# Kernel optimization log

Measured on AMD Instinct MI355X. Metric: run time of the kernel, lower is better.

## Reference

```python
import jax, jax.numpy as jnp
import numpy as np
from jax import lax

KS = 3
N = KS ** 3  # 27 kernel taps


def setup_inputs() -> dict:
    key = jax.random.key(0)
    k1, k2, k3 = jax.random.split(key, 3)
    B, Cin, Cout, D, H, W = 1, 32, 32, 32, 48, 48
    x = jax.random.normal(k1, (B, Cin, D, H, W), jnp.float32)
    # offset conv: 81 = 3*27 output channels, no bias (nn.Conv3d(..., bias=False))
    w_off = jax.random.normal(k2, (3 * N, Cin, KS, KS, KS), jnp.float32) * 0.01
    # deform conv kernel (bias defaults to None -> no bias)
    w_def = jax.random.normal(k3, (Cout, Cin, KS, KS, KS), jnp.float32) / np.sqrt(Cin * N)
    return {"x": x, "w_off": w_off, "w_def": w_def}


def _deform_block(x, w_off, w_def):
    B, C, D, H, W = x.shape
    dt = x.dtype

    # standard dense offset conv, padding=1
    offsets = lax.conv_general_dilated(
        x, w_off, (1, 1, 1), [(1, 1), (1, 1), (1, 1)],
        dimension_numbers=("NCDHW", "OIDHW", "NCDHW"))
    off = jnp.transpose(offsets, (0, 2, 3, 4, 1))  # (B,D,H,W,3N)
    od, oh, ow = off[..., :N], off[..., N:2 * N], off[..., 2 * N:]

    # zero-pad input (ConstantPad3d(1))
    xp = jnp.pad(x, ((0, 0), (0, 0), (1, 1), (1, 1), (1, 1)))
    Dp, Hp, Wp = D + 2, H + 2, W + 2

    # p_n: kernel grid offsets in (kd,kh,kw) row-major order, matching conv-weight layout
    r = jnp.arange(-(KS // 2), KS // 2 + 1, dtype=dt)
    pn = jnp.stack(jnp.meshgrid(r, r, r, indexing="ij"), 0).reshape(3, N)
    # p_0: centers in padded coordinates (1..D etc.)
    p0d = jnp.arange(1, D + 1, dtype=dt)[:, None, None, None]
    p0h = jnp.arange(1, H + 1, dtype=dt)[None, :, None, None]
    p0w = jnp.arange(1, W + 1, dtype=dt)[None, None, :, None]

    pd = p0d + pn[0] + od  # (B,D,H,W,N) sampling coords
    ph = p0h + pn[1] + oh
    pw = p0w + pn[2] + ow

    # integer corners (detached in original)
    fd = lax.stop_gradient(jnp.floor(pd))
    fh = lax.stop_gradient(jnp.floor(ph))
    fw = lax.stop_gradient(jnp.floor(pw))
    qd0 = jnp.clip(fd, 0, Dp - 1); qd1 = jnp.clip(fd + 1, 0, Dp - 1)
    qh0 = jnp.clip(fh, 0, Hp - 1); qh1 = jnp.clip(fh + 1, 0, Hp - 1)
    qw0 = jnp.clip(fw, 0, Wp - 1); qw1 = jnp.clip(fw + 1, 0, Wp - 1)

    # clip p to valid range (as in reference impl)
    pd = jnp.clip(pd, 0, Dp - 1)
    ph = jnp.clip(ph, 0, Hp - 1)
    pw = jnp.clip(pw, 0, Wp - 1)

    # trilinear weights per axis: g = 1 - |q - p|
    gd0 = 1 + (qd0 - pd); gd1 = 1 - (qd1 - pd)
    gh0 = 1 + (qh0 - ph); gh1 = 1 - (qh1 - ph)
    gw0 = 1 + (qw0 - pw); gw1 = 1 - (qw1 - pw)

    xf = xp.reshape(B, C, Dp * Hp * Wp)

    def gather(idd, ihh, iww):
        lin = ((idd.astype(jnp.int32) * Hp + ihh.astype(jnp.int32)) * Wp
               + iww.astype(jnp.int32)).reshape(B, 1, -1)
        v = jnp.take_along_axis(xf, jnp.broadcast_to(lin, (B, C, lin.shape[-1])), axis=2)
        return v.reshape(B, C, D, H, W, N)

    x_off = jnp.zeros((B, C, D, H, W, N), dt)
    for gd, idd in ((gd0, qd0), (gd1, qd1)):
        for gh, ihh in ((gh0, qh0), (gh1, qh1)):
            for gw, iww in ((gw0, qw0), (gw1, qw1)):
                x_off = x_off + (gd * gh * gw)[:, None] * gather(idd, ihh, iww)

    # stride-ks conv over reshaped x_offset == weighted sum over the N taps
    Cout = w_def.shape[0]
    out = jnp.einsum("bcdhwn,ocn->bodhw", x_off, w_def.reshape(Cout, C, N))
    return out


def reference(x, w_off, w_def):
    return _deform_block(x, w_off, w_def)
```

## Files before the change

### kernel.cpp

```cpp
#include <hip/hip_runtime.h>

typedef __attribute__((ext_vector_type(8))) short  short8;
typedef __attribute__((ext_vector_type(4))) float  f32x4;
typedef __attribute__((ext_vector_type(2))) float  f32x2;

#define CIN 32
#define COUT 32
#define DD 32
#define HH 48
#define WW 48
#define NTAP 27
#define SPATIAL (DD*HH*WW)

#define BP2_ELEMS (27*6*64*8)
#define OFF_WPK   ((size_t)BP2_ELEMS*2)
#define WPK_ELEMS (27*2*64*8)
#define OFF_XT    (OFF_WPK + (size_t)WPK_ELEMS*2)

#define SB0() __builtin_amdgcn_sched_barrier(0)

__device__ __forceinline__ unsigned short f2bf(float f) {
    union { float f; unsigned u; } v; v.f = f;
    unsigned r = v.u + 0x7FFFu + ((v.u >> 16) & 1u);
    return (unsigned short)(r >> 16);
}
__device__ __forceinline__ float bitsf(unsigned u) {
    union { unsigned u; float f; } v; v.u = u; return v.f;
}

__global__ __launch_bounds__(256) void wprep2_kernel(
        const float* __restrict__ w_off, unsigned short* __restrict__ Bp2)
{
    int i = blockIdx.x * 256 + threadIdx.x;
    if (i >= BP2_ELEMS) return;
    int e    = i & 7;
    int lane = (i >> 3) & 63;
    int j    = (i >> 9) % 6;
    int n    = i / (512 * 6);
    int col = lane & 15, kg = lane >> 4;
    int oc = j * 16 + col, c = kg * 8 + e;
    float v = (oc < 81) ? w_off[((size_t)oc * CIN + c) * NTAP + n] : 0.f;
    Bp2[i] = f2bf(v);
}

__global__ __launch_bounds__(256) void wdefprep_kernel(
        const float* __restrict__ w_def, unsigned short* __restrict__ wpk)
{
    int i = blockIdx.x * 256 + threadIdx.x;
    if (i >= WPK_ELEMS) return;
    int e    = i & 7;
    int lane = (i >> 3) & 63;
    int half = (i >> 9) & 1;
    int n    = i >> 10;
    int kg = lane >> 4, col = lane & 15;
    int c  = kg * 8 + e, oc = half * 16 + col;
    wpk[i] = f2bf(w_def[((size_t)oc * CIN + c) * NTAP + n]);
}

__global__ __launch_bounds__(256) void xtrans_kernel(
        const float* __restrict__ x, unsigned short* __restrict__ xT)
{
    __shared__ float t[CIN][65];
    const int p0 = blockIdx.x * 64;
    const int tid = threadIdx.x;
    const int tx = tid & 63, ty = tid >> 6;
    #pragma unroll
    for (int k = 0; k < 8; ++k) {
        int c = ty + k * 4;
        t[c][tx] = x[(size_t)c * SPATIAL + p0 + tx];
    }
    __syncthreads();
    const int pl = tid >> 2, cg = (tid & 3) * 8;
    short8 v;
    #pragma unroll
    for (int i = 0; i < 8; ++i) v[i] = (short)f2bf(t[cg + i][pl]);
    *(short8*)&xT[((size_t)(p0 + pl)) * 32 + cg] = v;
}

struct Gath {
    uint4 cw[8];
    float gg[8];
};

__device__ __forceinline__ void tap_issue(
        Gath& tb, const uint4* __restrict__ Xu,
        float od, float oh, float ow,
        int n, int d, int h, int w, int kg)
{
    float rd = (float)(n / 9) - 1.f;
    float rh = (float)((n / 3) % 3) - 1.f;
    float rw = (float)(n % 3) - 1.f;

    float pdp = (float)(d + 1) + rd + od;
    float php = (float)(h + 1) + rh + oh;
    float pwp = (float)(w + 1) + rw + ow;

    float fd = floorf(pdp), fh = floorf(php), fw = floorf(pwp);
    float qd0 = fminf(fmaxf(fd,       0.f), 33.f);
    float qd1 = fminf(fmaxf(fd + 1.f, 0.f), 33.f);
    float qh0 = fminf(fmaxf(fh,       0.f), 49.f);
    float qh1 = fminf(fmaxf(fh + 1.f, 0.f), 49.f);
    float qw0 = fminf(fmaxf(fw,       0.f), 49.f);
    float qw1 = fminf(fmaxf(fw + 1.f, 0.f), 49.f);
    float pcd = fminf(fmaxf(pdp, 0.f), 33.f);
    float pch = fminf(fmaxf(php, 0.f), 49.f);
    float pcw = fminf(fmaxf(pwp, 0.f), 49.f);

    float gd0 = 1.f + (qd0 - pcd), gd1 = 1.f - (qd1 - pcd);
    float gh0 = 1.f + (qh0 - pch), gh1 = 1.f - (qh1 - pch);
    float gw0 = 1.f + (qw0 - pcw), gw1 = 1.f - (qw1 - pcw);
    gd0 = (qd0 >= 1.f && qd0 <= 32.f) ? gd0 : 0.f;
    gd1 = (qd1 >= 1.f && qd1 <= 32.f) ? gd1 : 0.f;
    gh0 = (qh0 >= 1.f && qh0 <= 48.f) ? gh0 : 0.f;
    gh1 = (qh1 >= 1.f && qh1 <= 48.f) ? gh1 : 0.f;
    gw0 = (qw0 >= 1.f && qw0 <= 48.f) ? gw0 : 0.f;
    gw1 = (qw1 >= 1.f && qw1 <= 48.f) ? gw1 : 0.f;
    int zd0 = (int)fminf(fmaxf(qd0, 1.f), 32.f) - 1;
    int zd1 = (int)fminf(fmaxf(qd1, 1.f), 32.f) - 1;
    int zh0 = (int)fminf(fmaxf(qh0, 1.f), 48.f) - 1;
    int zh1 = (int)fminf(fmaxf(qh1, 1.f), 48.f) - 1;
    int zw0 = (int)fminf(fmaxf(qw0, 1.f), 48.f) - 1;
    int zw1 = (int)fminf(fmaxf(qw1, 1.f), 48.f) - 1;

    int bd0 = zd0 * 2304, bd1 = zd1 * 2304;
    int bh0 = zh0 * 48,   bh1 = zh1 * 48;
    float gdh00 = gd0 * gh0, gdh01 = gd0 * gh1;
    float gdh10 = gd1 * gh0, gdh11 = gd1 * gh1;

    tb.cw[0] = Xu[(size_t)(bd0 + bh0 + zw0) * 4 + kg];
    tb.cw[1] = Xu[(size_t)(bd0 + bh0 + zw1) * 4 + kg];
    tb.cw[2] = Xu[(size_t)(bd0 + bh1 + zw0) * 4 + kg];
    tb.cw[3] = Xu[(size_t)(bd0 + bh1 + zw1) * 4 + kg];
    tb.cw[4] = Xu[(size_t)(bd1 + bh0 + zw0) * 4 + kg];
    tb.cw[5] = Xu[(size_t)(bd1 + bh0 + zw1) * 4 + kg];
    tb.cw[6] = Xu[(size_t)(bd1 + bh1 + zw0) * 4 + kg];
    tb.cw[7] = Xu[(size_t)(bd1 + bh1 + zw1) * 4 + kg];

    tb.gg[0] = gdh00 * gw0;  tb.gg[1] = gdh00 * gw1;
    tb.gg[2] = gdh01 * gw0;  tb.gg[3] = gdh01 * gw1;
    tb.gg[4] = gdh10 * gw0;  tb.gg[5] = gdh10 * gw1;
    tb.gg[6] = gdh11 * gw0;  tb.gg[7] = gdh11 * gw1;
}

__device__ __forceinline__ void tap_consume(
        const Gath& tb, short8 b0, short8 b1, f32x4& acc0, f32x4& acc1)
{
    f32x2 xa0 = {0.f, 0.f}, xa1 = {0.f, 0.f};
    f32x2 xa2 = {0.f, 0.f}, xa3 = {0.f, 0.f};

    #pragma unroll
    for (int e = 0; e < 8; ++e) {
        uint4 cw = tb.cw[e];
        f32x2 g2 = {tb.gg[e], tb.gg[e]};
        f32x2 v0 = {bitsf(cw.x << 16), bitsf(cw.x & 0xFFFF0000u)};
        f32x2 v1 = {bitsf(cw.y << 16), bitsf(cw.y & 0xFFFF0000u)};
        f32x2 v2 = {bitsf(cw.z << 16), bitsf(cw.z & 0xFFFF0000u)};
        f32x2 v3 = {bitsf(cw.w << 16), bitsf(cw.w & 0xFFFF0000u)};
        asm("v_pk_fma_f32 %0, %1, %2, %0" : "+v"(xa0) : "v"(v0), "v"(g2));
        asm("v_pk_fma_f32 %0, %1, %2, %0" : "+v"(xa1) : "v"(v1), "v"(g2));
        asm("v_pk_fma_f32 %0, %1, %2, %0" : "+v"(xa2) : "v"(v2), "v"(g2));
        asm("v_pk_fma_f32 %0, %1, %2, %0" : "+v"(xa3) : "v"(v3), "v"(g2));
    }

    union { unsigned u[4]; short8 s; } av;
    asm("v_cvt_pk_bf16_f32 %0, %1, %2" : "=v"(av.u[0]) : "v"(xa0.x), "v"(xa0.y));
    asm("v_cvt_pk_bf16_f32 %0, %1, %2" : "=v"(av.u[1]) : "v"(xa1.x), "v"(xa1.y));
    asm("v_cvt_pk_bf16_f32 %0, %1, %2" : "=v"(av.u[2]) : "v"(xa2.x), "v"(xa2.y));
    asm("v_cvt_pk_bf16_f32 %0, %1, %2" : "=v"(av.u[3]) : "v"(xa3.x), "v"(xa3.y));

    acc0 = __builtin_amdgcn_mfma_f32_16x16x32_bf16(av.s, b0, acc0, 0, 0, 0);
    acc1 = __builtin_amdgcn_mfma_f32_16x16x32_bf16(av.s, b1, acc1, 0, 0, 0);
}

__global__ __launch_bounds__(192, 3) void fused_deform10(
        const unsigned short* __restrict__ xT,
        const unsigned short* __restrict__ Bp2,
        const unsigned short* __restrict__ wpk,
        float* __restrict__ out)
{
    __shared__ float offl[3][2][16][82];

    const int bid  = (int)blockIdx.x;
    const int sbid = (bid & 7) * 96 + (bid >> 3);

    const int tid  = threadIdx.x;
    const int lane = tid & 63, wv = tid >> 6;
    const int p0   = sbid * 96 + wv * 32;
    const int kg   = lane >> 4;
    const int row  = lane & 15;
    const int pos0 = p0 + row;
    const int pos1 = p0 + 16 + row;
    const int w0c = pos0 % WW, h0c = (pos0 / WW) % HH, d0c = pos0 / (WW * HH);
    const int w1c = pos1 % WW, h1c = (pos1 / WW) % HH, d1c = pos1 / (WW * HH);

    const uint4* Xu = (const uint4*)xT;
    const uint4* Bu = (const uint4*)Bp2;
    const uint4* Wu = (const uint4*)wpk;

    f32x4 cacc0[6], cacc1[6];
    #pragma unroll
    for (int j = 0; j < 6; ++j) {
        cacc0[j] = (f32x4){0.f, 0.f, 0.f, 0.f};
        cacc1[j] = (f32x4){0.f, 0.f, 0.f, 0.f};
    }

    {
        #pragma unroll 1
        for (int n = 0; n < NTAP; ++n) {
            int td = n / 9, th = (n / 3) % 3, tw = n % 3;
            int dis = (td - 1) * 2304 + (th - 1) * 48 + (tw - 1);
            int v0 = ((unsigned)(d0c + td - 1) < DD) & ((unsigned)(h0c + th - 1) < HH)
                   & ((unsigned)(w0c + tw - 1) < WW);
            int v1 = ((unsigned)(d1c + td - 1) < DD) & ((unsigned)(h1c + th - 1) < HH)
                   & ((unsigned)(w1c + tw - 1) < WW);
            uint4 a0 = Xu[(size_t)(v0 ? pos0 + dis : pos0) * 4 + kg];
            uint4 a1 = Xu[(size_t)(v1 ? pos1 + dis : pos1) * 4 + kg];
            uint4 wt[6];
            #pragma unroll
            for (int j = 0; j < 6; ++j)
                wt[j] = Bu[(size_t)(n * 6 + j) * 64 + lane];
            SB0();
            if (!v0) { a0.x = 0; a0.y = 0; a0.z = 0; a0.w = 0; }
            if (!v1) { a1.x = 0; a1.y = 0; a1.z = 0; a1.w = 0; }
            union { uint4 u; short8 s; } av0, av1, b;
            av0.u = a0; av1.u = a1;
            #pragma unroll
            for (int j = 0; j < 6; ++j) {
                b.u = wt[j];
                cacc0[j] = __builtin_amdgcn_mfma_f32_16x16x32_bf16(av0.s, b.s, cacc0[j], 0, 0, 0);
                cacc1[j] = __builtin_amdgcn_mfma_f32_16x16x32_bf16(av1.s, b.s, cacc1[j], 0, 0, 0);
            }
        }
    }

    #pragma unroll
    for (int j = 0; j < 6; ++j) {
        #pragma unroll
        for (int r = 0; r < 4; ++r) {
            int col = j * 16 + row;
            if (col < 81) {
                offl[wv][0][kg * 4 + r][col] = cacc0[j][r];
                offl[wv][1][kg * 4 + r][col] = cacc1[j][r];
            }
        }
    }
    __syncthreads();

    const float* ol0 = &offl[wv][0][row][0];
    const float* ol1 = &offl[wv][1][row][0];

    f32x4 acc00 = {0.f, 0.f, 0.f, 0.f}, acc01 = {0.f, 0.f, 0.f, 0.f};
    f32x4 acc10 = {0.f, 0.f, 0.f, 0.f}, acc11 = {0.f, 0.f, 0.f, 0.f};

    {
        Gath g0, g1;
        #pragma unroll 1
        for (int n = 0; n < NTAP; ++n) {
            uint4 wbu0 = Wu[(size_t)(n * 2 + 0) * 64 + lane];
            uint4 wbu1 = Wu[(size_t)(n * 2 + 1) * 64 + lane];
            tap_issue(g0, Xu, ol0[n], ol0[27 + n], ol0[54 + n], n, d0c, h0c, w0c, kg);
            SB0();
            tap_issue(g1, Xu, ol1[n], ol1[27 + n], ol1[54 + n], n, d1c, h1c, w1c, kg);
            SB0();
            union { uint4 u; short8 s; } b0, b1;
            b0.u = wbu0; b1.u = wbu1;
            tap_consume(g0, b0.s, b1.s, acc00, acc01);
            tap_consume(g1, b0.s, b1.s, acc10, acc11);
        }
    }

    const int pb0 = p0 + kg * 4;
    const int pb1 = p0 + 16 + kg * 4;
    *(f32x4*)&out[(size_t)row        * SPATIAL + pb0] = acc00;
    *(f32x4*)&out[(size_t)(16 + row) * SPATIAL + pb0] = acc01;
    *(f32x4*)&out[(size_t)row        * SPATIAL + pb1] = acc10;
    *(f32x4*)&out[(size_t)(16 + row) * SPATIAL + pb1] = acc11;
}

extern "C" void kernel_launch(void* const* d_in, const int* in_sizes, int n_in,
                              void* d_out, int out_size, void* d_ws, size_t ws_size,
                              hipStream_t stream)
{
    const float* x     = (const float*)d_in[0];
    const float* w_off = (const float*)d_in[1];
    const float* w_def = (const float*)d_in[2];
    float* out = (float*)d_out;

    unsigned short* Bp2 = (unsigned short*)((char*)d_ws);
    unsigned short* wpk = (unsigned short*)((char*)d_ws + OFF_WPK);
    unsigned short* xT  = (unsigned short*)((char*)d_ws + OFF_XT);

    wprep2_kernel<<<(BP2_ELEMS + 255) / 256, 256, 0, stream>>>(w_off, Bp2);
    wdefprep_kernel<<<(WPK_ELEMS + 255) / 256, 256, 0, stream>>>(w_def, wpk);
    xtrans_kernel<<<SPATIAL / 64, 256, 0, stream>>>(x, xT);
    fused_deform10<<<SPATIAL / 96, 192, 0, stream>>>(xT, Bp2, wpk, out);
}
```

Measured before the change: 118.4 us.

## Process four 16-position tiles per wave to reuse weight loads and deepen gather pipelining

Each wave now handles 64 output positions instead of 32, and blocks shrink to two waves, so there are 576 blocks of 128 threads. The offset-conv and deform weight fragments loaded per tap are reused across four MFMA tiles instead of two. The gather loop is software-pipelined so one tile's issue overlaps another tile's consume. The cost is more accumulator registers (cacc arrays double) and lower occupancy, with launch bounds changed to (128,2).

```diff
diff --git a/kernel.cpp b/kernel.cpp
--- a/kernel.cpp
+++ b/kernel.cpp
@@ -172,36 +172,43 @@
     acc1 = __builtin_amdgcn_mfma_f32_16x16x32_bf16(av.s, b1, acc1, 0, 0, 0);
 }
 
-__global__ __launch_bounds__(192, 3) void fused_deform10(
+__global__ __launch_bounds__(128, 2) void fused_deform11(
         const unsigned short* __restrict__ xT,
         const unsigned short* __restrict__ Bp2,
         const unsigned short* __restrict__ wpk,
         float* __restrict__ out)
 {
-    __shared__ float offl[3][2][16][82];
+    __shared__ float offl[2][4][16][82];
 
     const int bid  = (int)blockIdx.x;
-    const int sbid = (bid & 7) * 96 + (bid >> 3);
+    const int sbid = (bid & 7) * 72 + (bid >> 3);
 
     const int tid  = threadIdx.x;
     const int lane = tid & 63, wv = tid >> 6;
-    const int p0   = sbid * 96 + wv * 32;
+    const int p0   = sbid * 128 + wv * 64;
     const int kg   = lane >> 4;
     const int row  = lane & 15;
-    const int pos0 = p0 + row;
-    const int pos1 = p0 + 16 + row;
-    const int w0c = pos0 % WW, h0c = (pos0 / WW) % HH, d0c = pos0 / (WW * HH);
-    const int w1c = pos1 % WW, h1c = (pos1 / WW) % HH, d1c = pos1 / (WW * HH);
+
+    int posv[4], dv[4], hv[4], wvv[4];
+    #pragma unroll
+    for (int t = 0; t < 4; ++t) {
+        posv[t] = p0 + t * 16 + row;
+        wvv[t]  = posv[t] % WW;
+        hv[t]   = (posv[t] / WW) % HH;
+        dv[t]   = posv[t] / (WW * HH);
+    }
 
     const uint4* Xu = (const uint4*)xT;
     const uint4* Bu = (const uint4*)Bp2;
     const uint4* Wu = (const uint4*)wpk;
 
-    f32x4 cacc0[6], cacc1[6];
+    f32x4 cacc0[6], cacc1[6], cacc2[6], cacc3[6];
     #pragma unroll
     for (int j = 0; j < 6; ++j) {
         cacc0[j] = (f32x4){0.f, 0.f, 0.f, 0.f};
         cacc1[j] = (f32x4){0.f, 0.f, 0.f, 0.f};
+        cacc2[j] = (f32x4){0.f, 0.f, 0.f, 0.f};
+        cacc3[j] = (f32x4){0.f, 0.f, 0.f, 0.f};
     }
 
     {
@@ -209,38 +216,46 @@
         for (int n = 0; n < NTAP; ++n) {
             int td = n / 9, th = (n / 3) % 3, tw = n % 3;
             int dis = (td - 1) * 2304 + (th - 1) * 48 + (tw - 1);
-            int v0 = ((unsigned)(d0c + td - 1) < DD) & ((unsigned)(h0c + th - 1) < HH)
-                   & ((unsigned)(w0c + tw - 1) < WW);
-            int v1 = ((unsigned)(d1c + td - 1) < DD) & ((unsigned)(h1c + th - 1) < HH)
-                   & ((unsigned)(w1c + tw - 1) < WW);
-            uint4 a0 = Xu[(size_t)(v0 ? pos0 + dis : pos0) * 4 + kg];
-            uint4 a1 = Xu[(size_t)(v1 ? pos1 + dis : pos1) * 4 + kg];
+            uint4 a[4];
+            int vmask[4];
+            #pragma unroll
+            for (int t = 0; t < 4; ++t) {
+                vmask[t] = ((unsigned)(dv[t] + td - 1) < DD)
+                         & ((unsigned)(hv[t] + th - 1) < HH)
+                         & ((unsigned)(wvv[t] + tw - 1) < WW);
+                a[t] = Xu[(size_t)(vmask[t] ? posv[t] + dis : posv[t]) * 4 + kg];
+            }
             uint4 wt[6];
             #pragma unroll
             for (int j = 0; j < 6; ++j)
                 wt[j] = Bu[(size_t)(n * 6 + j) * 64 + lane];
             SB0();
-            if (!v0) { a0.x = 0; a0.y = 0; a0.z = 0; a0.w = 0; }
-            if (!v1) { a1.x = 0; a1.y = 0; a1.z = 0; a1.w = 0; }
-            union { uint4 u; short8 s; } av0, av1, b;
-            av0.u = a0; av1.u = a1;
+            #pragma unroll
+            for (int t = 0; t < 4; ++t)
+                if (!vmask[t]) { a[t].x = 0; a[t].y = 0; a[t].z = 0; a[t].w = 0; }
+            union { uint4 u; short8 s; } av0, av1, av2, av3, b;
+            av0.u = a[0]; av1.u = a[1]; av2.u = a[2]; av3.u = a[3];
             #pragma unroll
             for (int j = 0; j < 6; ++j) {
                 b.u = wt[j];
                 cacc0[j] = __builtin_amdgcn_mfma_f32_16x16x32_bf16(av0.s, b.s, cacc0[j], 0, 0, 0);
                 cacc1[j] = __builtin_amdgcn_mfma_f32_16x16x32_bf16(av1.s, b.s, cacc1[j], 0, 0, 0);
+                cacc2[j] = __builtin_amdgcn_mfma_f32_16x16x32_bf16(av2.s, b.s, cacc2[j], 0, 0, 0);
+                cacc3[j] = __builtin_amdgcn_mfma_f32_16x16x32_bf16(av3.s, b.s, cacc3[j], 0, 0, 0);
             }
         }
     }
 
     #pragma unroll
     for (int j = 0; j < 6; ++j) {
-        #pragma unroll
-        for (int r = 0; r < 4; ++r) {
-            int col = j * 16 + row;
-            if (col < 81) {
+        int col = j * 16 + row;
+        if (col < 81) {
+            #pragma unroll
+            for (int r = 0; r < 4; ++r) {
                 offl[wv][0][kg * 4 + r][col] = cacc0[j][r];
                 offl[wv][1][kg * 4 + r][col] = cacc1[j][r];
+                offl[wv][2][kg * 4 + r][col] = cacc2[j][r];
+                offl[wv][3][kg * 4 + r][col] = cacc3[j][r];
             }
         }
     }
@@ -248,33 +263,47 @@
 
     const float* ol0 = &offl[wv][0][row][0];
     const float* ol1 = &offl[wv][1][row][0];
-
-    f32x4 acc00 = {0.f, 0.f, 0.f, 0.f}, acc01 = {0.f, 0.f, 0.f, 0.f};
-    f32x4 acc10 = {0.f, 0.f, 0.f, 0.f}, acc11 = {0.f, 0.f, 0.f, 0.f};
+    const float* ol2 = &offl[wv][2][row][0];
+    const float* ol3 = &offl[wv][3][row][0];
+
+    f32x4 acc00 = {0.f,0.f,0.f,0.f}, acc01 = {0.f,0.f,0.f,0.f};
+    f32x4 acc10 = {0.f,0.f,0.f,0.f}, acc11 = {0.f,0.f,0.f,0.f};
+    f32x4 acc20 = {0.f,0.f,0.f,0.f}, acc21 = {0.f,0.f,0.f,0.f};
+    f32x4 acc30 = {0.f,0.f,0.f,0.f}, acc31 = {0.f,0.f,0.f,0.f};
 
     {
-        Gath g0, g1;
+        Gath gA, gB;
         #pragma unroll 1
         for (int n = 0; n < NTAP; ++n) {
             uint4 wbu0 = Wu[(size_t)(n * 2 + 0) * 64 + lane];
             uint4 wbu1 = Wu[(size_t)(n * 2 + 1) * 64 + lane];
-            tap_issue(g0, Xu, ol0[n], ol0[27 + n], ol0[54 + n], n, d0c, h0c, w0c, kg);
-            SB0();
-            tap_issue(g1, Xu, ol1[n], ol1[27 + n], ol1[54 + n], n, d1c, h1c, w1c, kg);
-            SB0();
             union { uint4 u; short8 s; } b0, b1;
             b0.u = wbu0; b1.u = wbu1;
-            tap_consume(g0, b0.s, b1.s, acc00, acc01);
-            tap_consume(g1, b0.s, b1.s, acc10, acc11);
+
+            tap_issue(gA, Xu, ol0[n], ol0[27 + n], ol0[54 + n], n, dv[0], hv[0], wvv[0], kg);
+            SB0();
+            tap_issue(gB, Xu, ol1[n], ol1[27 + n], ol1[54 + n], n, dv[1], hv[1], wvv[1], kg);
+            SB0();
+            tap_consume(gA, b0.s, b1.s, acc00, acc01);
+            tap_issue(gA, Xu, ol2[n], ol2[27 + n], ol2[54 + n], n, dv[2], hv[2], wvv[2], kg);
+            SB0();
+            tap_consume(gB, b0.s, b1.s, acc10, acc11);
+            tap_issue(gB, Xu, ol3[n], ol3[27 + n], ol3[54 + n], n, dv[3], hv[3], wvv[3], kg);
+            SB0();
+            tap_consume(gA, b0.s, b1.s, acc20, acc21);
+            tap_consume(gB, b0.s, b1.s, acc30, acc31);
         }
     }
 
     const int pb0 = p0 + kg * 4;
-    const int pb1 = p0 + 16 + kg * 4;
-    *(f32x4*)&out[(size_t)row        * SPATIAL + pb0] = acc00;
-    *(f32x4*)&out[(size_t)(16 + row) * SPATIAL + pb0] = acc01;
-    *(f32x4*)&out[(size_t)row        * SPATIAL + pb1] = acc10;
-    *(f32x4*)&out[(size_t)(16 + row) * SPATIAL + pb1] = acc11;
+    *(f32x4*)&out[(size_t)row        * SPATIAL + pb0]      = acc00;
+    *(f32x4*)&out[(size_t)(16 + row) * SPATIAL + pb0]      = acc01;
+    *(f32x4*)&out[(size_t)row        * SPATIAL + pb0 + 16] = acc10;
+    *(f32x4*)&out[(size_t)(16 + row) * SPATIAL + pb0 + 16] = acc11;
+    *(f32x4*)&out[(size_t)row        * SPATIAL + pb0 + 32] = acc20;
+    *(f32x4*)&out[(size_t)(16 + row) * SPATIAL + pb0 + 32] = acc21;
+    *(f32x4*)&out[(size_t)row        * SPATIAL + pb0 + 48] = acc30;
+    *(f32x4*)&out[(size_t)(16 + row) * SPATIAL + pb0 + 48] = acc31;
 }
 
 extern "C" void kernel_launch(void* const* d_in, const int* in_sizes, int n_in,
@@ -293,5 +322,5 @@
     wprep2_kernel<<<(BP2_ELEMS + 255) / 256, 256, 0, stream>>>(w_off, Bp2);
     wdefprep_kernel<<<(WPK_ELEMS + 255) / 256, 256, 0, stream>>>(w_def, wpk);
     xtrans_kernel<<<SPATIAL / 64, 256, 0, stream>>>(x, xT);
-    fused_deform10<<<SPATIAL / 96, 192, 0, stream>>>(xT, Bp2, wpk, out);
-}
+    fused_deform11<<<SPATIAL / 128, 128, 0, stream>>>(xT, Bp2, wpk, out);
+}
```

New measurement: 142.5 us. +20.3%, slower.
